# Kernel optimization log

Hardware: AMD Instinct MI355X
Metric: run time of the kernel (lower is better)

Reference implementation:

```python
import jax, jax.numpy as jnp
import numpy as np

N = 128          # number of samples; P = N*(N-1)/2 = 8128 pairs
D = 8128         # feature dim; must equal P for the module's einsum('ij,ji->i')
EPS = 1e-12

# static pair indices matching the original loop order: for i, for j < i
_II, _JJ = np.tril_indices(N, k=-1)  # each length P = 8128


def setup_inputs() -> dict:
    key = jax.random.key(0)
    k1, k2 = jax.random.split(key)
    S_real = jax.random.normal(k1, (N, D), dtype=jnp.float32)
    S_fake = jax.random.normal(k2, (N, D), dtype=jnp.float32)
    return {"S_real": S_real, "S_fake": S_fake}


def _cosine_loss(real, fake, eps):
    # real, fake: [P, D] with P == D
    norm_real = jnp.linalg.norm(real, axis=1, keepdims=True)
    norm_fake = jnp.linalg.norm(fake, axis=1, keepdims=True)
    mat_real = jnp.maximum(real / norm_real, eps)
    mat_fake = jnp.maximum(fake / norm_fake, eps)
    # einsum('ij,ji->i') then sum == total sum of mat_fake * mat_real.T
    return jnp.einsum('ij,ji->i', mat_fake, mat_real).sum()


def reference(S_real, S_fake):
    # vectorized pairwise differences, same order as the python double loop
    v_real = S_real[_II] - S_real[_JJ]   # [P, D]
    v_fake = S_fake[_II] - S_fake[_JJ]   # [P, D]
    return _cosine_loss(v_real, v_fake, EPS)
```

## Files before the change

kernel.cpp:

```cpp
#include <hip/hip_runtime.h>

#define NS   128
#define D_   8128
#define DP_  8192
#define P_   8128
#define PP   8192
#define EPSV 1e-12f
#define NT   127
#define KS8  8

typedef __attribute__((ext_vector_type(8))) short short8;
typedef __attribute__((ext_vector_type(4))) float f32x4;
typedef __attribute__((ext_vector_type(2))) float f32x2;

static __device__ __forceinline__ unsigned short f32_to_bf16_rne(float f) {
    unsigned int u = __float_as_uint(f);
    return (unsigned short)((u + 0x7fffu + ((u >> 16) & 1u)) >> 16);
}
static __device__ __forceinline__ unsigned int pack2_bf16(float a, float b) {
    return (unsigned int)f32_to_bf16_rne(a) | ((unsigned int)f32_to_bf16_rne(b) << 16);
}
static __device__ __forceinline__ float bf16_lo(unsigned int u) { return __uint_as_float(u << 16); }
static __device__ __forceinline__ float bf16_hi(unsigned int u) { return __uint_as_float(u & 0xffff0000u); }

__global__ void cvt_pad(const float* __restrict__ Sr, const float* __restrict__ Sf,
                        unsigned short* __restrict__ Sr16, unsigned short* __restrict__ Sf16) {
    int idx = blockIdx.x * 256 + threadIdx.x;
    int m   = idx >> 17;
    int rem = idx & 131071;
    int row = rem >> 10;
    int c8  = rem & 1023;
    const float* __restrict__ S = m ? Sf : Sr;
    unsigned short* __restrict__ Dst = m ? Sf16 : Sr16;
    uint4 o;
    if (c8 < 1016) {
        const float* src = S + (size_t)row * D_ + 8 * c8;
        float4 v0 = *(const float4*)src;
        float4 v1 = *(const float4*)(src + 4);
        o.x = pack2_bf16(v0.x, v0.y);
        o.y = pack2_bf16(v0.z, v0.w);
        o.z = pack2_bf16(v1.x, v1.y);
        o.w = pack2_bf16(v1.z, v1.w);
    } else {
        o.x = 0u; o.y = 0u; o.z = 0u; o.w = 0u;
    }
    *(uint4*)(Dst + (size_t)row * DP_ + 8 * c8) = o;
}

__global__ void __launch_bounds__(64)
gram_direct(const unsigned short* __restrict__ Sr16, const unsigned short* __restrict__ Sf16,
            float* __restrict__ Gpart8) {
    int tile = blockIdx.x;
    int I = tile >> 3, J = tile & 7;
    int m = blockIdx.y;
    int s = blockIdx.z;
    const unsigned short* __restrict__ S = m ? Sf16 : Sr16;
    float* __restrict__ out = Gpart8 + ((size_t)s * 2 + m) * (NS * NS);

    int l  = threadIdx.x;
    int lr = l & 15;
    int kf = (l >> 4) * 8;

    const unsigned short* pa = S + (size_t)(I * 16 + lr) * DP_ + kf;
    const unsigned short* pb = S + (size_t)(J * 16 + lr) * DP_ + kf;

    f32x4 acc = (f32x4)0.f;
    int ks0 = s * 32;
    int ks1 = (ks0 + 32 < 254) ? ks0 + 32 : 254;
    #pragma unroll 4
    for (int ks = ks0; ks < ks1; ++ks) {
        short8 a = *(const short8*)(pa + ks * 32);
        short8 b = *(const short8*)(pb + ks * 32);
        acc = __builtin_amdgcn_mfma_f32_16x16x32_bf16(a, b, acc, 0, 0, 0);
    }
    int rbase = I * 16 + (l >> 4) * 4;
    int col   = J * 16 + lr;
    #pragma unroll
    for (int r = 0; r < 4; ++r)
        out[(rbase + r) * NS + col] = acc[r];
}

__global__ void norm_finish(const float* __restrict__ Gpart8,
                            float* __restrict__ inv_nr, float* __restrict__ inv_nf,
                            int* __restrict__ opi, int* __restrict__ opj) {
    int p = blockIdx.x * 256 + threadIdx.x;
    if (p >= PP) return;
    if (p >= P_) {
        inv_nr[p] = 0.f;
        inv_nf[p] = 0.f;
        opi[p] = 0;
        opj[p] = 0;
        return;
    }
    int i = (int)((1.0f + sqrtf(8.0f * (float)p + 1.0f)) * 0.5f);
    while (i * (i - 1) / 2 > p) --i;
    while ((i + 1) * i / 2 <= p) ++i;
    int j = p - i * (i - 1) / 2;

    float rii = 0.f, rjj = 0.f, rij = 0.f;
    float fii = 0.f, fjj = 0.f, fij = 0.f;
    #pragma unroll
    for (int s = 0; s < KS8; ++s) {
        const float* g0 = Gpart8 + ((size_t)s * 2 + 0) * (NS * NS);
        const float* g1 = Gpart8 + ((size_t)s * 2 + 1) * (NS * NS);
        rii += g0[i * NS + i]; rjj += g0[j * NS + j]; rij += g0[i * NS + j];
        fii += g1[i * NS + i]; fjj += g1[j * NS + j]; fij += g1[i * NS + j];
    }
    inv_nr[p] = rsqrtf(fmaxf(rii + rjj - 2.f * rij, 1e-30f));
    inv_nf[p] = rsqrtf(fmaxf(fii + fjj - 2.f * fij, 1e-30f));
    opi[p] = i * DP_;
    opj[p] = j * DP_;
}

__global__ void __launch_bounds__(256, 6)
tile8_kernel(const unsigned short* __restrict__ Sr16, const unsigned short* __restrict__ Sf16,
             const float* __restrict__ inv_nr, const float* __restrict__ inv_nf,
             const int* __restrict__ opi, const int* __restrict__ opj,
             float* __restrict__ partials) {
    __shared__ float Rl[16 * 260];
    __shared__ int   sOi[64], sOj[64];
    __shared__ float sInvF[64];
    __shared__ float wsum[4];

    int t  = threadIdx.x;
    int p0 = blockIdx.x * 64;
    int q0 = blockIdx.y * 64;

    if (t < 64) {
        int p = p0 + t;
        sOi[t]   = opi[p];
        sOj[t]   = opj[p];
        sInvF[t] = inv_nf[p];
    }

    #pragma unroll
    for (int s = 0; s < 2; ++s) {
        int task = t + 256 * s;
        int q = task >> 3, slot = task & 7;
        int gq = q0 + q;
        int oiq = opi[gq], ojq = opj[gq];
        float invr = inv_nr[gq];
        uint4 ua = *(const uint4*)(Sr16 + oiq + p0 + 8 * slot);
        uint4 ub = *(const uint4*)(Sr16 + ojq + p0 + 8 * slot);
        f32x2 inv2; inv2.x = invr; inv2.y = invr;
        f32x2 A, B, V;
        f32x4 w0, w1;
        A.x = bf16_lo(ua.x); A.y = bf16_hi(ua.x);
        B.x = bf16_lo(ub.x); B.y = bf16_hi(ub.x);
        V = (A - B) * inv2;
        w0.x = fmaxf(V.x, EPSV); w0.y = fmaxf(V.y, EPSV);
        A.x = bf16_lo(ua.y); A.y = bf16_hi(ua.y);
        B.x = bf16_lo(ub.y); B.y = bf16_hi(ub.y);
        V = (A - B) * inv2;
        w0.z = fmaxf(V.x, EPSV); w0.w = fmaxf(V.y, EPSV);
        A.x = bf16_lo(ua.z); A.y = bf16_hi(ua.z);
        B.x = bf16_lo(ub.z); B.y = bf16_hi(ub.z);
        V = (A - B) * inv2;
        w1.x = fmaxf(V.x, EPSV); w1.y = fmaxf(V.y, EPSV);
        A.x = bf16_lo(ua.w); A.y = bf16_hi(ua.w);
        B.x = bf16_lo(ub.w); B.y = bf16_hi(ub.w);
        V = (A - B) * inv2;
        w1.z = fmaxf(V.x, EPSV); w1.w = fmaxf(V.y, EPSV);
        float* dst = &Rl[(q >> 2) * 260 + (q & 3) * 64 + 8 * slot];
        *(f32x4*)dst = w0;
        *(f32x4*)(dst + 4) = w1;
    }
    __syncthreads();

    int qg = t & 15;
    int pg = t >> 4;
    int4   oi4 = *(const int4*)&sOi[4 * pg];
    int4   oj4 = *(const int4*)&sOj[4 * pg];
    float4 if4 = *(const float4*)&sInvF[4 * pg];
    int oiA[4] = {oi4.x, oi4.y, oi4.z, oi4.w};
    int ojA[4] = {oj4.x, oj4.y, oj4.z, oj4.w};
    float ifA[4] = {if4.x, if4.y, if4.z, if4.w};

    f32x2 F[4][2];
    #pragma unroll
    for (int r = 0; r < 4; ++r) {
        uint2 ua = *(const uint2*)(Sf16 + oiA[r] + q0 + 4 * qg);
        uint2 ub = *(const uint2*)(Sf16 + ojA[r] + q0 + 4 * qg);
        f32x2 inv2; inv2.x = ifA[r]; inv2.y = ifA[r];
        f32x2 A0, A1, B0, B1;
        A0.x = bf16_lo(ua.x); A0.y = bf16_hi(ua.x);
        A1.x = bf16_lo(ua.y); A1.y = bf16_hi(ua.y);
        B0.x = bf16_lo(ub.x); B0.y = bf16_hi(ub.x);
        B1.x = bf16_lo(ub.y); B1.y = bf16_hi(ub.y);
        f32x2 V0 = (A0 - B0) * inv2;
        f32x2 V1 = (A1 - B1) * inv2;
        F[r][0].x = fmaxf(V0.x, EPSV); F[r][0].y = fmaxf(V0.y, EPSV);
        F[r][1].x = fmaxf(V1.x, EPSV); F[r][1].y = fmaxf(V1.y, EPSV);
    }

    float acc = 0.f;
    const float* rbase = &Rl[qg * 260 + 4 * pg];
    #pragma unroll
    for (int k = 0; k < 4; ++k) {
        f32x4 Rv = *(const f32x4*)(rbase + k * 64);
        float fq0 = (k & 1) ? F[0][k >> 1].y : F[0][k >> 1].x;
        float fq1 = (k & 1) ? F[1][k >> 1].y : F[1][k >> 1].x;
        float fq2 = (k & 1) ? F[2][k >> 1].y : F[2][k >> 1].x;
        float fq3 = (k & 1) ? F[3][k >> 1].y : F[3][k >> 1].x;
        acc += fq0 * Rv.x + fq1 * Rv.y + fq2 * Rv.z + fq3 * Rv.w;
    }

    #pragma unroll
    for (int off = 32; off > 0; off >>= 1) acc += __shfl_down(acc, off, 64);
    if ((t & 63) == 0) wsum[t >> 6] = acc;
    __syncthreads();
    if (t == 0) partials[blockIdx.y * 128 + blockIdx.x] = wsum[0] + wsum[1] + wsum[2] + wsum[3];
}

__global__ void norms_kernel(const float* __restrict__ Sr, const float* __restrict__ Sf,
                             float* __restrict__ inv_nr, float* __restrict__ inv_nf,
                             int* __restrict__ opi, int* __restrict__ opj) {
    int p = blockIdx.x;
    int i = (int)((1.0f + sqrtf(8.0f * (float)p + 1.0f)) * 0.5f);
    while (i * (i - 1) / 2 > p) --i;
    while ((i + 1) * i / 2 <= p) ++i;
    int j = p - i * (i - 1) / 2;

    const float4* ri = (const float4*)(Sr + (size_t)i * D_);
    const float4* rj = (const float4*)(Sr + (size_t)j * D_);
    const float4* fi = (const float4*)(Sf + (size_t)i * D_);
    const float4* fj = (const float4*)(Sf + (size_t)j * D_);

    float sr = 0.f, sf = 0.f;
    for (int d = threadIdx.x; d < D_ / 4; d += 256) {
        float4 a = ri[d], b = rj[d];
        float dx = a.x - b.x, dy = a.y - b.y, dz = a.z - b.z, dw = a.w - b.w;
        sr += dx * dx + dy * dy + dz * dz + dw * dw;
        float4 c2 = fi[d], e = fj[d];
        dx = c2.x - e.x; dy = c2.y - e.y; dz = c2.z - e.z; dw = c2.w - e.w;
        sf += dx * dx + dy * dy + dz * dz + dw * dw;
    }
    #pragma unroll
    for (int off = 32; off > 0; off >>= 1) {
        sr += __shfl_down(sr, off, 64);
        sf += __shfl_down(sf, off, 64);
    }
    __shared__ float wr[4], wf[4];
    int wave = threadIdx.x >> 6;
    if ((threadIdx.x & 63) == 0) { wr[wave] = sr; wf[wave] = sf; }
    __syncthreads();
    if (threadIdx.x == 0) {
        inv_nr[p] = 1.0f / sqrtf(wr[0] + wr[1] + wr[2] + wr[3]);
        inv_nf[p] = 1.0f / sqrtf(wf[0] + wf[1] + wf[2] + wf[3]);
        opi[p] = i * D_;
        opj[p] = j * D_;
    }
}

__global__ void __launch_bounds__(256, 6)
tile3_kernel(const float* __restrict__ Sr, const float* __restrict__ Sf,
             const float* __restrict__ inv_nr, const float* __restrict__ inv_nf,
             const int* __restrict__ opi, const int* __restrict__ opj,
             float* __restrict__ partials) {
    __shared__ float Rt[64][65];
    __shared__ int   sIp[64], sJp[64];
    __shared__ float sInvF[64];
    __shared__ float wsum[4];

    int t  = threadIdx.x;
    int p0 = blockIdx.x * 64, q0 = blockIdx.y * 64;

    if (t < 64) {
        int p = p0 + t;
        sIp[t]   = opi[p];
        sJp[t]   = opj[p];
        sInvF[t] = inv_nf[p];
    }
    {
        int c  = t & 15;
        int qr = t >> 4;
        #pragma unroll
        for (int pass = 0; pass < 4; ++pass) {
            int qq = qr + 16 * pass;
            int q  = q0 + qq;
            int oi = opi[q], oj = opj[q];
            float invr = inv_nr[q];
            const float4 a = *(const float4*)(Sr + oi + p0 + 4 * c);
            const float4 b = *(const float4*)(Sr + oj + p0 + 4 * c);
            Rt[4 * c + 0][qq] = fmaxf((a.x - b.x) * invr, EPSV);
            Rt[4 * c + 1][qq] = fmaxf((a.y - b.y) * invr, EPSV);
            Rt[4 * c + 2][qq] = fmaxf((a.z - b.z) * invr, EPSV);
            Rt[4 * c + 3][qq] = fmaxf((a.w - b.w) * invr, EPSV);
        }
    }
    __syncthreads();

    int qg = t & 15;
    int pg = t >> 4;
    float ax = 0.f, ay = 0.f, az = 0.f, aw = 0.f;
    #pragma unroll
    for (int pp = 0; pp < 4; ++pp) {
        int prow = pg + 16 * pp;
        int oi = sIp[prow], oj = sJp[prow];
        float invf = sInvF[prow];
        const float4 fa = *(const float4*)(Sf + oi + q0 + 4 * qg);
        const float4 fb = *(const float4*)(Sf + oj + q0 + 4 * qg);
        const float4 r  = *(const float4*)&Rt[prow][4 * qg];
        ax += fmaxf((fa.x - fb.x) * invf, EPSV) * r.x;
        ay += fmaxf((fa.y - fb.y) * invf, EPSV) * r.y;
        az += fmaxf((fa.z - fb.z) * invf, EPSV) * r.z;
        aw += fmaxf((fa.w - fb.w) * invf, EPSV) * r.w;
    }
    float acc = (ax + ay) + (az + aw);

    #pragma unroll
    for (int off = 32; off > 0; off >>= 1) acc += __shfl_down(acc, off, 64);
    int w = t >> 6;
    if ((t & 63) == 0) wsum[w] = acc;
    __syncthreads();
    if (t == 0) partials[blockIdx.y * NT + blockIdx.x] = wsum[0] + wsum[1] + wsum[2] + wsum[3];
}

__global__ void reduce_kernel(const float* __restrict__ partials, int n, float* __restrict__ out) {
    float s = 0.f;
    for (int idx = threadIdx.x; idx < n; idx += 1024) s += partials[idx];
    #pragma unroll
    for (int off = 32; off > 0; off >>= 1) s += __shfl_down(s, off, 64);
    __shared__ float wbuf[16];
    int wave = threadIdx.x >> 6;
    if ((threadIdx.x & 63) == 0) wbuf[wave] = s;
    __syncthreads();
    if (threadIdx.x == 0) {
        float tot = 0.f;
        #pragma unroll
        for (int k = 0; k < 16; ++k) tot += wbuf[k];
        out[0] = tot;
    }
}

extern "C" void kernel_launch(void* const* d_in, const int* in_sizes, int n_in,
                              void* d_out, int out_size, void* d_ws, size_t ws_size,
                              hipStream_t stream) {
    const float* Sr = (const float*)d_in[0];
    const float* Sf = (const float*)d_in[1];
    float* out = (float*)d_out;

    char* w = (char*)d_ws;
    unsigned short* Sr16 = (unsigned short*)w;   w += (size_t)NS * DP_ * 2;
    unsigned short* Sf16 = (unsigned short*)w;   w += (size_t)NS * DP_ * 2;
    float* inv_nr = (float*)w;                   w += (size_t)PP * 4;
    float* inv_nf = (float*)w;                   w += (size_t)PP * 4;
    int*   opi    = (int*)w;                     w += (size_t)PP * 4;
    int*   opj    = (int*)w;                     w += (size_t)PP * 4;
    float* tpart  = (float*)w;                   w += (size_t)16384 * 4;
    float* Gpart8 = (float*)w;                   w += (size_t)KS8 * 2 * NS * NS * 4;
    size_t need = (size_t)(w - (char*)d_ws);

    if (ws_size >= need) {
        cvt_pad<<<1024, 256, 0, stream>>>(Sr, Sf, Sr16, Sf16);
        dim3 gg(64, 2, KS8);
        gram_direct<<<gg, 64, 0, stream>>>(Sr16, Sf16, Gpart8);
        norm_finish<<<32, 256, 0, stream>>>(Gpart8, inv_nr, inv_nf, opi, opj);
        dim3 grid(128, 128);
        tile8_kernel<<<grid, 256, 0, stream>>>(Sr16, Sf16, inv_nr, inv_nf, opi, opj, tpart);
        reduce_kernel<<<1, 1024, 0, stream>>>(tpart, 16384, out);
    } else {
        norms_kernel<<<P_, 256, 0, stream>>>(Sr, Sf, inv_nr, inv_nf, opi, opj);
        dim3 grid(NT, NT);
        tile3_kernel<<<grid, 256, 0, stream>>>(Sr, Sf, inv_nr, inv_nf, opi, opj, tpart);
        reduce_kernel<<<1, 1024, 0, stream>>>(tpart, NT * NT, out);
    }
}
```

Measured before the change: 60.67 us.

## Stage fake-sample column slab in LDS and loop over 16 p-tiles per block

The tile kernel now loads all 128 rows of the bf16 fake matrix for the block's 64-column q slab into shared memory once. Each block then iterates over 16 p-tiles, building the fake pair differences from LDS instead of gathering them from global memory for every tile. The grid shrinks from 128x128 to 8x128 blocks, so far fewer partials need reducing. The cost is an extra 16KB of LDS per block, lower launch-bounds occupancy, and a serial loop with two barriers per step, which reduces parallelism to 1024 blocks.

```diff
diff --git a/kernel.cpp b/kernel.cpp
--- a/kernel.cpp
+++ b/kernel.cpp
@@ -112,104 +112,114 @@
     opj[p] = j * DP_;
 }
 
-__global__ void __launch_bounds__(256, 6)
-tile8_kernel(const unsigned short* __restrict__ Sr16, const unsigned short* __restrict__ Sf16,
+__global__ void __launch_bounds__(256, 4)
+tile9_kernel(const unsigned short* __restrict__ Sr16, const unsigned short* __restrict__ Sf16,
              const float* __restrict__ inv_nr, const float* __restrict__ inv_nf,
              const int* __restrict__ opi, const int* __restrict__ opj,
              float* __restrict__ partials) {
+    __shared__ unsigned short Sfl[128 * 64];
     __shared__ float Rl[16 * 260];
-    __shared__ int   sOi[64], sOj[64];
+    __shared__ int   sIi[64], sIj[64];
     __shared__ float sInvF[64];
     __shared__ float wsum[4];
 
     int t  = threadIdx.x;
-    int p0 = blockIdx.x * 64;
     int q0 = blockIdx.y * 64;
 
-    if (t < 64) {
-        int p = p0 + t;
-        sOi[t]   = opi[p];
-        sOj[t]   = opj[p];
-        sInvF[t] = inv_nf[p];
-    }
-
-    #pragma unroll
-    for (int s = 0; s < 2; ++s) {
+    #pragma unroll
+    for (int s = 0; s < 4; ++s) {
         int task = t + 256 * s;
-        int q = task >> 3, slot = task & 7;
-        int gq = q0 + q;
-        int oiq = opi[gq], ojq = opj[gq];
-        float invr = inv_nr[gq];
-        uint4 ua = *(const uint4*)(Sr16 + oiq + p0 + 8 * slot);
-        uint4 ub = *(const uint4*)(Sr16 + ojq + p0 + 8 * slot);
-        f32x2 inv2; inv2.x = invr; inv2.y = invr;
-        f32x2 A, B, V;
-        f32x4 w0, w1;
-        A.x = bf16_lo(ua.x); A.y = bf16_hi(ua.x);
-        B.x = bf16_lo(ub.x); B.y = bf16_hi(ub.x);
-        V = (A - B) * inv2;
-        w0.x = fmaxf(V.x, EPSV); w0.y = fmaxf(V.y, EPSV);
-        A.x = bf16_lo(ua.y); A.y = bf16_hi(ua.y);
-        B.x = bf16_lo(ub.y); B.y = bf16_hi(ub.y);
-        V = (A - B) * inv2;
-        w0.z = fmaxf(V.x, EPSV); w0.w = fmaxf(V.y, EPSV);
-        A.x = bf16_lo(ua.z); A.y = bf16_hi(ua.z);
-        B.x = bf16_lo(ub.z); B.y = bf16_hi(ub.z);
-        V = (A - B) * inv2;
-        w1.x = fmaxf(V.x, EPSV); w1.y = fmaxf(V.y, EPSV);
-        A.x = bf16_lo(ua.w); A.y = bf16_hi(ua.w);
-        B.x = bf16_lo(ub.w); B.y = bf16_hi(ub.w);
-        V = (A - B) * inv2;
-        w1.z = fmaxf(V.x, EPSV); w1.w = fmaxf(V.y, EPSV);
-        float* dst = &Rl[(q >> 2) * 260 + (q & 3) * 64 + 8 * slot];
-        *(f32x4*)dst = w0;
-        *(f32x4*)(dst + 4) = w1;
-    }
-    __syncthreads();
+        int row = task >> 3, oct = task & 7;
+        *(uint4*)&Sfl[row * 64 + 8 * oct] =
+            *(const uint4*)(Sf16 + (size_t)row * DP_ + q0 + 8 * oct);
+    }
 
     int qg = t & 15;
     int pg = t >> 4;
-    int4   oi4 = *(const int4*)&sOi[4 * pg];
-    int4   oj4 = *(const int4*)&sOj[4 * pg];
-    float4 if4 = *(const float4*)&sInvF[4 * pg];
-    int oiA[4] = {oi4.x, oi4.y, oi4.z, oi4.w};
-    int ojA[4] = {oj4.x, oj4.y, oj4.z, oj4.w};
-    float ifA[4] = {if4.x, if4.y, if4.z, if4.w};
-
-    f32x2 F[4][2];
-    #pragma unroll
-    for (int r = 0; r < 4; ++r) {
-        uint2 ua = *(const uint2*)(Sf16 + oiA[r] + q0 + 4 * qg);
-        uint2 ub = *(const uint2*)(Sf16 + ojA[r] + q0 + 4 * qg);
-        f32x2 inv2; inv2.x = ifA[r]; inv2.y = ifA[r];
-        f32x2 A0, A1, B0, B1;
-        A0.x = bf16_lo(ua.x); A0.y = bf16_hi(ua.x);
-        A1.x = bf16_lo(ua.y); A1.y = bf16_hi(ua.y);
-        B0.x = bf16_lo(ub.x); B0.y = bf16_hi(ub.x);
-        B1.x = bf16_lo(ub.y); B1.y = bf16_hi(ub.y);
-        f32x2 V0 = (A0 - B0) * inv2;
-        f32x2 V1 = (A1 - B1) * inv2;
-        F[r][0].x = fmaxf(V0.x, EPSV); F[r][0].y = fmaxf(V0.y, EPSV);
-        F[r][1].x = fmaxf(V1.x, EPSV); F[r][1].y = fmaxf(V1.y, EPSV);
-    }
-
     float acc = 0.f;
-    const float* rbase = &Rl[qg * 260 + 4 * pg];
-    #pragma unroll
-    for (int k = 0; k < 4; ++k) {
-        f32x4 Rv = *(const f32x4*)(rbase + k * 64);
-        float fq0 = (k & 1) ? F[0][k >> 1].y : F[0][k >> 1].x;
-        float fq1 = (k & 1) ? F[1][k >> 1].y : F[1][k >> 1].x;
-        float fq2 = (k & 1) ? F[2][k >> 1].y : F[2][k >> 1].x;
-        float fq3 = (k & 1) ? F[3][k >> 1].y : F[3][k >> 1].x;
-        acc += fq0 * Rv.x + fq1 * Rv.y + fq2 * Rv.z + fq3 * Rv.w;
+
+    for (int step = 0; step < 16; ++step) {
+        int p0 = (blockIdx.x * 16 + step) * 64;
+
+        if (t < 64) {
+            int p = p0 + t;
+            sIi[t]   = opi[p] >> 13;
+            sIj[t]   = opj[p] >> 13;
+            sInvF[t] = inv_nf[p];
+        }
+
+        #pragma unroll
+        for (int s = 0; s < 2; ++s) {
+            int task = t + 256 * s;
+            int q = task >> 3, slot = task & 7;
+            int gq = q0 + q;
+            int oiq = opi[gq], ojq = opj[gq];
+            float invr = inv_nr[gq];
+            uint4 ua = *(const uint4*)(Sr16 + oiq + p0 + 8 * slot);
+            uint4 ub = *(const uint4*)(Sr16 + ojq + p0 + 8 * slot);
+            f32x2 inv2; inv2.x = invr; inv2.y = invr;
+            f32x2 A, B, V;
+            f32x4 w0, w1;
+            A.x = bf16_lo(ua.x); A.y = bf16_hi(ua.x);
+            B.x = bf16_lo(ub.x); B.y = bf16_hi(ub.x);
+            V = (A - B) * inv2;
+            w0.x = fmaxf(V.x, EPSV); w0.y = fmaxf(V.y, EPSV);
+            A.x = bf16_lo(ua.y); A.y = bf16_hi(ua.y);
+            B.x = bf16_lo(ub.y); B.y = bf16_hi(ub.y);
+            V = (A - B) * inv2;
+            w0.z = fmaxf(V.x, EPSV); w0.w = fmaxf(V.y, EPSV);
+            A.x = bf16_lo(ua.z); A.y = bf16_hi(ua.z);
+            B.x = bf16_lo(ub.z); B.y = bf16_hi(ub.z);
+            V = (A - B) * inv2;
+            w1.x = fmaxf(V.x, EPSV); w1.y = fmaxf(V.y, EPSV);
+            A.x = bf16_lo(ua.w); A.y = bf16_hi(ua.w);
+            B.x = bf16_lo(ub.w); B.y = bf16_hi(ub.w);
+            V = (A - B) * inv2;
+            w1.z = fmaxf(V.x, EPSV); w1.w = fmaxf(V.y, EPSV);
+            float* dst = &Rl[(q >> 2) * 260 + (q & 3) * 64 + 8 * slot];
+            *(f32x4*)dst = w0;
+            *(f32x4*)(dst + 4) = w1;
+        }
+        __syncthreads();
+
+        f32x2 F[4][2];
+        #pragma unroll
+        for (int r = 0; r < 4; ++r) {
+            int prow = 4 * pg + r;
+            int ii = sIi[prow], jj = sIj[prow];
+            float invf = sInvF[prow];
+            uint2 ua = *(const uint2*)&Sfl[ii * 64 + 4 * qg];
+            uint2 ub = *(const uint2*)&Sfl[jj * 64 + 4 * qg];
+            f32x2 inv2; inv2.x = invf; inv2.y = invf;
+            f32x2 A0, A1, B0, B1;
+            A0.x = bf16_lo(ua.x); A0.y = bf16_hi(ua.x);
+            A1.x = bf16_lo(ua.y); A1.y = bf16_hi(ua.y);
+            B0.x = bf16_lo(ub.x); B0.y = bf16_hi(ub.x);
+            B1.x = bf16_lo(ub.y); B1.y = bf16_hi(ub.y);
+            f32x2 V0 = (A0 - B0) * inv2;
+            f32x2 V1 = (A1 - B1) * inv2;
+            F[r][0].x = fmaxf(V0.x, EPSV); F[r][0].y = fmaxf(V0.y, EPSV);
+            F[r][1].x = fmaxf(V1.x, EPSV); F[r][1].y = fmaxf(V1.y, EPSV);
+        }
+
+        const float* rbase = &Rl[qg * 260 + 4 * pg];
+        #pragma unroll
+        for (int k = 0; k < 4; ++k) {
+            f32x4 Rv = *(const f32x4*)(rbase + k * 64);
+            float fq0 = (k & 1) ? F[0][k >> 1].y : F[0][k >> 1].x;
+            float fq1 = (k & 1) ? F[1][k >> 1].y : F[1][k >> 1].x;
+            float fq2 = (k & 1) ? F[2][k >> 1].y : F[2][k >> 1].x;
+            float fq3 = (k & 1) ? F[3][k >> 1].y : F[3][k >> 1].x;
+            acc += fq0 * Rv.x + fq1 * Rv.y + fq2 * Rv.z + fq3 * Rv.w;
+        }
+        __syncthreads();
     }
 
     #pragma unroll
     for (int off = 32; off > 0; off >>= 1) acc += __shfl_down(acc, off, 64);
     if ((t & 63) == 0) wsum[t >> 6] = acc;
     __syncthreads();
-    if (t == 0) partials[blockIdx.y * 128 + blockIdx.x] = wsum[0] + wsum[1] + wsum[2] + wsum[3];
+    if (t == 0) partials[blockIdx.y * 8 + blockIdx.x] = wsum[0] + wsum[1] + wsum[2] + wsum[3];
 }
 
 __global__ void norms_kernel(const float* __restrict__ Sr, const float* __restrict__ Sf,
@@ -356,9 +366,9 @@
         dim3 gg(64, 2, KS8);
         gram_direct<<<gg, 64, 0, stream>>>(Sr16, Sf16, Gpart8);
         norm_finish<<<32, 256, 0, stream>>>(Gpart8, inv_nr, inv_nf, opi, opj);
-        dim3 grid(128, 128);
-        tile8_kernel<<<grid, 256, 0, stream>>>(Sr16, Sf16, inv_nr, inv_nf, opi, opj, tpart);
-        reduce_kernel<<<1, 1024, 0, stream>>>(tpart, 16384, out);
+        dim3 grid(8, 128);
+        tile9_kernel<<<grid, 256, 0, stream>>>(Sr16, Sf16, inv_nr, inv_nf, opi, opj, tpart);
+        reduce_kernel<<<1, 1024, 0, stream>>>(tpart, 1024, out);
     } else {
         norms_kernel<<<P_, 256, 0, stream>>>(Sr, Sf, inv_nr, inv_nf, opi, opj);
         dim3 grid(NT, NT);
```

Measured after the change: 56.01 us. 1.08x faster.

## Stage fake-sample column slab in LDS and loop over eight p-tiles per block

Applied to the files above, without the earlier changes.

Replaces the 64x64-tile kernel with one that loads a 128x64 bf16 slab of the fake matrix into XOR-swizzled shared memory once per q-tile. Each block then iterates over eight p-tiles, building fake pair-differences from LDS and real pair-differences directly from global memory in registers. The grid shrinks eightfold and the final reduction takes fewer partials. This amortizes the fake-side gathers and the block launch overhead, but drops the shared-memory staging of the real tile, so each thread now issues more scattered global loads per step.

```diff
diff --git a/kernel.cpp b/kernel.cpp
--- a/kernel.cpp
+++ b/kernel.cpp
@@ -11,7 +11,6 @@
 
 typedef __attribute__((ext_vector_type(8))) short short8;
 typedef __attribute__((ext_vector_type(4))) float f32x4;
-typedef __attribute__((ext_vector_type(2))) float f32x2;
 
 static __device__ __forceinline__ unsigned short f32_to_bf16_rne(float f) {
     unsigned int u = __float_as_uint(f);
@@ -22,6 +21,15 @@
 }
 static __device__ __forceinline__ float bf16_lo(unsigned int u) { return __uint_as_float(u << 16); }
 static __device__ __forceinline__ float bf16_hi(unsigned int u) { return __uint_as_float(u & 0xffff0000u); }
+
+static __device__ __forceinline__ f32x4 gen4(uint2 a, uint2 b, float inv) {
+    f32x4 r;
+    r.x = fmaxf((bf16_lo(a.x) - bf16_lo(b.x)) * inv, EPSV);
+    r.y = fmaxf((bf16_hi(a.x) - bf16_hi(b.x)) * inv, EPSV);
+    r.z = fmaxf((bf16_lo(a.y) - bf16_lo(b.y)) * inv, EPSV);
+    r.w = fmaxf((bf16_hi(a.y) - bf16_hi(b.y)) * inv, EPSV);
+    return r;
+}
 
 __global__ void cvt_pad(const float* __restrict__ Sr, const float* __restrict__ Sf,
                         unsigned short* __restrict__ Sr16, unsigned short* __restrict__ Sf16) {
@@ -113,103 +121,82 @@
 }
 
 __global__ void __launch_bounds__(256, 6)
-tile8_kernel(const unsigned short* __restrict__ Sr16, const unsigned short* __restrict__ Sf16,
-             const float* __restrict__ inv_nr, const float* __restrict__ inv_nf,
-             const int* __restrict__ opi, const int* __restrict__ opj,
-             float* __restrict__ partials) {
-    __shared__ float Rl[16 * 260];
-    __shared__ int   sOi[64], sOj[64];
-    __shared__ float sInvF[64];
+tile10_kernel(const unsigned short* __restrict__ Sr16, const unsigned short* __restrict__ Sf16,
+              const float* __restrict__ inv_nr, const float* __restrict__ inv_nf,
+              const int* __restrict__ opi, const int* __restrict__ opj,
+              float* __restrict__ partials) {
+    __shared__ unsigned short Sfl[128 * 64];
     __shared__ float wsum[4];
 
     int t  = threadIdx.x;
-    int p0 = blockIdx.x * 64;
     int q0 = blockIdx.y * 64;
-
-    if (t < 64) {
-        int p = p0 + t;
-        sOi[t]   = opi[p];
-        sOj[t]   = opj[p];
-        sInvF[t] = inv_nf[p];
-    }
-
-    #pragma unroll
-    for (int s = 0; s < 2; ++s) {
+    int pg = t & 15;
+    int qg = t >> 4;
+
+    #pragma unroll
+    for (int s = 0; s < 8; ++s) {
         int task = t + 256 * s;
-        int q = task >> 3, slot = task & 7;
-        int gq = q0 + q;
-        int oiq = opi[gq], ojq = opj[gq];
-        float invr = inv_nr[gq];
-        uint4 ua = *(const uint4*)(Sr16 + oiq + p0 + 8 * slot);
-        uint4 ub = *(const uint4*)(Sr16 + ojq + p0 + 8 * slot);
-        f32x2 inv2; inv2.x = invr; inv2.y = invr;
-        f32x2 A, B, V;
-        f32x4 w0, w1;
-        A.x = bf16_lo(ua.x); A.y = bf16_hi(ua.x);
-        B.x = bf16_lo(ub.x); B.y = bf16_hi(ub.x);
-        V = (A - B) * inv2;
-        w0.x = fmaxf(V.x, EPSV); w0.y = fmaxf(V.y, EPSV);
-        A.x = bf16_lo(ua.y); A.y = bf16_hi(ua.y);
-        B.x = bf16_lo(ub.y); B.y = bf16_hi(ub.y);
-        V = (A - B) * inv2;
-        w0.z = fmaxf(V.x, EPSV); w0.w = fmaxf(V.y, EPSV);
-        A.x = bf16_lo(ua.z); A.y = bf16_hi(ua.z);
-        B.x = bf16_lo(ub.z); B.y = bf16_hi(ub.z);
-        V = (A - B) * inv2;
-        w1.x = fmaxf(V.x, EPSV); w1.y = fmaxf(V.y, EPSV);
-        A.x = bf16_lo(ua.w); A.y = bf16_hi(ua.w);
-        B.x = bf16_lo(ub.w); B.y = bf16_hi(ub.w);
-        V = (A - B) * inv2;
-        w1.z = fmaxf(V.x, EPSV); w1.w = fmaxf(V.y, EPSV);
-        float* dst = &Rl[(q >> 2) * 260 + (q & 3) * 64 + 8 * slot];
-        *(f32x4*)dst = w0;
-        *(f32x4*)(dst + 4) = w1;
-    }
-    __syncthreads();
-
-    int qg = t & 15;
-    int pg = t >> 4;
-    int4   oi4 = *(const int4*)&sOi[4 * pg];
-    int4   oj4 = *(const int4*)&sOj[4 * pg];
-    float4 if4 = *(const float4*)&sInvF[4 * pg];
-    int oiA[4] = {oi4.x, oi4.y, oi4.z, oi4.w};
-    int ojA[4] = {oj4.x, oj4.y, oj4.z, oj4.w};
-    float ifA[4] = {if4.x, if4.y, if4.z, if4.w};
-
-    f32x2 F[4][2];
-    #pragma unroll
-    for (int r = 0; r < 4; ++r) {
-        uint2 ua = *(const uint2*)(Sf16 + oiA[r] + q0 + 4 * qg);
-        uint2 ub = *(const uint2*)(Sf16 + ojA[r] + q0 + 4 * qg);
-        f32x2 inv2; inv2.x = ifA[r]; inv2.y = ifA[r];
-        f32x2 A0, A1, B0, B1;
-        A0.x = bf16_lo(ua.x); A0.y = bf16_hi(ua.x);
-        A1.x = bf16_lo(ua.y); A1.y = bf16_hi(ua.y);
-        B0.x = bf16_lo(ub.x); B0.y = bf16_hi(ub.x);
-        B1.x = bf16_lo(ub.y); B1.y = bf16_hi(ub.y);
-        f32x2 V0 = (A0 - B0) * inv2;
-        f32x2 V1 = (A1 - B1) * inv2;
-        F[r][0].x = fmaxf(V0.x, EPSV); F[r][0].y = fmaxf(V0.y, EPSV);
-        F[r][1].x = fmaxf(V1.x, EPSV); F[r][1].y = fmaxf(V1.y, EPSV);
-    }
+        int row = task >> 4, slot = task & 15;
+        uint2 v = *(const uint2*)(Sf16 + (size_t)row * DP_ + q0 + 4 * slot);
+        *(uint2*)&Sfl[row * 64 + 4 * (slot ^ (row & 15))] = v;
+    }
+
+    int q4 = q0 + 4 * qg;
+    int4   oiq   = *(const int4*)&opi[q4];
+    int4   ojq   = *(const int4*)&opj[q4];
+    float4 invr4 = *(const float4*)&inv_nr[q4];
+    __syncthreads();
 
     float acc = 0.f;
-    const float* rbase = &Rl[qg * 260 + 4 * pg];
-    #pragma unroll
-    for (int k = 0; k < 4; ++k) {
-        f32x4 Rv = *(const f32x4*)(rbase + k * 64);
-        float fq0 = (k & 1) ? F[0][k >> 1].y : F[0][k >> 1].x;
-        float fq1 = (k & 1) ? F[1][k >> 1].y : F[1][k >> 1].x;
-        float fq2 = (k & 1) ? F[2][k >> 1].y : F[2][k >> 1].x;
-        float fq3 = (k & 1) ? F[3][k >> 1].y : F[3][k >> 1].x;
-        acc += fq0 * Rv.x + fq1 * Rv.y + fq2 * Rv.z + fq3 * Rv.w;
+    for (int step = 0; step < 8; ++step) {
+        int pb = ((blockIdx.x * 8 + step) << 6) + 4 * pg;
+
+        int4   pio   = *(const int4*)&opi[pb];
+        int4   pjo   = *(const int4*)&opj[pb];
+        float4 invf4 = *(const float4*)&inv_nf[pb];
+
+        uint2 ru0 = *(const uint2*)(Sr16 + oiq.x + pb);
+        uint2 rv0 = *(const uint2*)(Sr16 + ojq.x + pb);
+        uint2 ru1 = *(const uint2*)(Sr16 + oiq.y + pb);
+        uint2 rv1 = *(const uint2*)(Sr16 + ojq.y + pb);
+        uint2 ru2 = *(const uint2*)(Sr16 + oiq.z + pb);
+        uint2 rv2 = *(const uint2*)(Sr16 + ojq.z + pb);
+        uint2 ru3 = *(const uint2*)(Sr16 + oiq.w + pb);
+        uint2 rv3 = *(const uint2*)(Sr16 + ojq.w + pb);
+
+        int ii0 = pio.x >> 13, jj0 = pjo.x >> 13;
+        int ii1 = pio.y >> 13, jj1 = pjo.y >> 13;
+        int ii2 = pio.z >> 13, jj2 = pjo.z >> 13;
+        int ii3 = pio.w >> 13, jj3 = pjo.w >> 13;
+        uint2 fu0 = *(const uint2*)&Sfl[ii0 * 64 + 4 * (qg ^ (ii0 & 15))];
+        uint2 fv0 = *(const uint2*)&Sfl[jj0 * 64 + 4 * (qg ^ (jj0 & 15))];
+        uint2 fu1 = *(const uint2*)&Sfl[ii1 * 64 + 4 * (qg ^ (ii1 & 15))];
+        uint2 fv1 = *(const uint2*)&Sfl[jj1 * 64 + 4 * (qg ^ (jj1 & 15))];
+        uint2 fu2 = *(const uint2*)&Sfl[ii2 * 64 + 4 * (qg ^ (ii2 & 15))];
+        uint2 fv2 = *(const uint2*)&Sfl[jj2 * 64 + 4 * (qg ^ (jj2 & 15))];
+        uint2 fu3 = *(const uint2*)&Sfl[ii3 * 64 + 4 * (qg ^ (ii3 & 15))];
+        uint2 fv3 = *(const uint2*)&Sfl[jj3 * 64 + 4 * (qg ^ (jj3 & 15))];
+
+        f32x4 R0 = gen4(ru0, rv0, invr4.x);
+        f32x4 R1 = gen4(ru1, rv1, invr4.y);
+        f32x4 R2 = gen4(ru2, rv2, invr4.z);
+        f32x4 R3 = gen4(ru3, rv3, invr4.w);
+        f32x4 F0 = gen4(fu0, fv0, invf4.x);
+        f32x4 F1 = gen4(fu1, fv1, invf4.y);
+        f32x4 F2 = gen4(fu2, fv2, invf4.z);
+        f32x4 F3 = gen4(fu3, fv3, invf4.w);
+
+        acc += F0.x * R0.x + F0.y * R1.x + F0.z * R2.x + F0.w * R3.x;
+        acc += F1.x * R0.y + F1.y * R1.y + F1.z * R2.y + F1.w * R3.y;
+        acc += F2.x * R0.z + F2.y * R1.z + F2.z * R2.z + F2.w * R3.z;
+        acc += F3.x * R0.w + F3.y * R1.w + F3.z * R2.w + F3.w * R3.w;
     }
 
     #pragma unroll
     for (int off = 32; off > 0; off >>= 1) acc += __shfl_down(acc, off, 64);
     if ((t & 63) == 0) wsum[t >> 6] = acc;
     __syncthreads();
-    if (t == 0) partials[blockIdx.y * 128 + blockIdx.x] = wsum[0] + wsum[1] + wsum[2] + wsum[3];
+    if (t == 0) partials[blockIdx.y * 16 + blockIdx.x] = wsum[0] + wsum[1] + wsum[2] + wsum[3];
 }
 
 __global__ void norms_kernel(const float* __restrict__ Sr, const float* __restrict__ Sf,
@@ -356,9 +343,9 @@
         dim3 gg(64, 2, KS8);
         gram_direct<<<gg, 64, 0, stream>>>(Sr16, Sf16, Gpart8);
         norm_finish<<<32, 256, 0, stream>>>(Gpart8, inv_nr, inv_nf, opi, opj);
-        dim3 grid(128, 128);
-        tile8_kernel<<<grid, 256, 0, stream>>>(Sr16, Sf16, inv_nr, inv_nf, opi, opj, tpart);
-        reduce_kernel<<<1, 1024, 0, stream>>>(tpart, 16384, out);
+        dim3 grid(16, 128);
+        tile10_kernel<<<grid, 256, 0, stream>>>(Sr16, Sf16, inv_nr, inv_nf, opi, opj, tpart);
+        reduce_kernel<<<1, 1024, 0, stream>>>(tpart, 2048, out);
     } else {
         norms_kernel<<<P_, 256, 0, stream>>>(Sr, Sf, inv_nr, inv_nf, opi, opj);
         dim3 grid(NT, NT);
```

Measured after the change: 54.74 us. -9.8%, faster.
